# Kernel optimization log

Hardware: AMD Instinct MI355X
Metric: run time of the kernel (lower is better)

## Reference

```python
import jax, jax.numpy as jnp
import numpy as np

H, W = 512, 512          # image_size
N = 10000                # num gaussians (point cloud size)
NUM_VIEWS = 4
PATCH = 40               # original uses arange(v-20, v+20) -> 40px window


def setup_inputs() -> dict:
    key = jax.random.key(0)
    ks = jax.random.split(key, 6)
    means = jax.random.normal(ks[0], (N, 3), dtype=jnp.float32) * 0.5
    log_scales = jnp.log(0.1) + 0.1 * jax.random.normal(ks[1], (N, 3), dtype=jnp.float32)
    q = jax.random.normal(ks[2], (N, 4), dtype=jnp.float32)
    quats = q / jnp.linalg.norm(q, axis=1, keepdims=True)
    shs = jax.random.normal(ks[3], (N, 3, 16), dtype=jnp.float32) * 0.1  # (sh_degree+1)^2 = 16
    opacities = jnp.full((N, 1), 0.5, dtype=jnp.float32)
    # Camera poses: small yaw sweep looking at the origin from z=+5 so points project in-frame.
    poses = []
    for a in np.linspace(-0.1, 0.1, NUM_VIEWS):
        Rm = np.array([[np.cos(a), 0.0, np.sin(a)],
                       [0.0, 1.0, 0.0],
                       [-np.sin(a), 0.0, np.cos(a)]], dtype=np.float32)
        P = np.eye(4, dtype=np.float32)
        P[:3, :3] = Rm
        P[:3, 3] = np.array([0.0, 0.0, 5.0], dtype=np.float32)
        poses.append(P)
    poses = jnp.asarray(np.stack(poses))
    intrinsics = jnp.asarray(np.array([[500.0, 0.0, 256.0],
                                       [0.0, 500.0, 256.0],
                                       [0.0, 0.0, 1.0]], dtype=np.float32))
    return {"poses": poses, "intrinsics": intrinsics, "means": means,
            "log_scales": log_scales, "quats": quats, "shs": shs, "opacities": opacities}


def _quat_to_mat(q):
    # q: (N,4) wxyz -> (N,3,3), same formula as the torch module
    w, x, y, z = q[:, 0], q[:, 1], q[:, 2], q[:, 3]
    r0 = jnp.stack([1 - 2 * (y * y + z * z), 2 * (x * y - w * z), 2 * (x * z + w * y)], -1)
    r1 = jnp.stack([2 * (x * y + w * z), 1 - 2 * (x * x + z * z), 2 * (y * z - w * x)], -1)
    r2 = jnp.stack([2 * (x * z - w * y), 2 * (y * z + w * x), 1 - 2 * (x * x + y * y)], -1)
    return jnp.stack([r0, r1, r2], -2)


def _render_view(pose, K, means, log_scales, quats, shs, opacities):
    Rm = pose[:3, :3]
    t = pose[:3, 3]
    p_cam = means @ Rm.T + t                      # (N,3)
    p_proj = p_cam @ K.T                          # (N,3)
    uv = p_proj[:, :2] / (p_proj[:, 2:3] + 1e-8)  # (N,2)
    u = jnp.trunc(uv[:, 0]).astype(jnp.int32)     # int(uv) truncation as in python int()
    v = jnp.trunc(uv[:, 1]).astype(jnp.int32)
    valid = (p_cam[:, 2] >= 0.1) & (u >= 0) & (u < W) & (v >= 0) & (v < H)

    scales = jnp.exp(log_scales)                  # (N,3); module uses scale (not scale^2)
    Rg = _quat_to_mat(quats)                      # (N,3,3)
    cov = jnp.einsum('nij,nj,nkj->nik', Rg, scales, Rg)  # R diag(s) R^T
    a, b = cov[:, 0, 0], cov[:, 0, 1]
    c, d = cov[:, 1, 0], cov[:, 1, 1]
    det = a * d - b * c
    inv = jnp.stack([jnp.stack([d, -b], -1), jnp.stack([-c, a], -1)], -2) / det[:, None, None]  # inverse of cov[:2,:2]

    off = jnp.arange(PATCH, dtype=jnp.int32) - PATCH // 2  # -20..19, matches arange(v-20, v+20)
    yy = jnp.broadcast_to(v[:, None, None] + off[None, :, None], (N, PATCH, PATCH))
    xx = jnp.broadcast_to(u[:, None, None] + off[None, None, :], (N, PATCH, PATCH))
    pos = jnp.stack([xx, yy], -1).astype(jnp.float32) - uv[:, None, None, :]  # (N,40,40,2)
    expo = -0.5 * jnp.einsum('nyxi,nij,nyxj->nyx', pos, inv, pos)
    g = jnp.exp(jnp.clip(expo, -10.0, 0.0))

    inb = (yy >= 0) & (yy < H) & (xx >= 0) & (xx < W)
    mask = valid[:, None, None] & inb & (g > 0.001)

    color = jax.nn.sigmoid(shs[:, :, 0])          # (N,3)
    op = jax.nn.sigmoid(opacities)                # (N,1)
    contrib = jnp.where(mask, g, 0.0)[..., None] * (op * color)[:, None, None, :]  # (N,40,40,3)

    image = jnp.zeros((H, W, 3), jnp.float32)
    image = image.at[jnp.clip(yy, 0, H - 1), jnp.clip(xx, 0, W - 1)].add(contrib)
    return image


def reference(poses, intrinsics, means, log_scales, quats, shs, opacities):
    # loop over a small fixed number of views (matches forward's per-view loop)
    imgs = [_render_view(poses[i], intrinsics, means, log_scales, quats, shs, opacities)
            for i in range(NUM_VIEWS)]
    return jnp.stack(imgs)  # (num_views, H, W, 3)
```

## Files before the change

kernel.cpp:

```cpp
#include <hip/hip_runtime.h>

#define IMG_H 512
#define IMG_W 512
#define NGAUSS 10000
#define N_VIEWS 4
#define PATCH 40
#define TOTAL_G (N_VIEWS * NGAUSS)

#define QMAX 13.815511f

struct __align__(16) Desc {
    float uvx, uvy, i00, i01;
    float i11, w0, w1, w2;
    int xlo, ylo, wx, area;
};

__global__ __launch_bounds__(256) void gs_prep_kernel(
    const float* __restrict__ poses,
    const float* __restrict__ Km,
    const float* __restrict__ means,
    const float* __restrict__ log_scales,
    const float* __restrict__ quats,
    const float* __restrict__ shs,
    const float* __restrict__ opac,
    Desc* __restrict__ descs,
    float4* __restrict__ out4, int n4)
{
    const int tid = blockIdx.x * 256 + threadIdx.x;

    for (int i = tid; i < n4; i += gridDim.x * 256)
        out4[i] = make_float4(0.f, 0.f, 0.f, 0.f);

    if (tid >= TOTAL_G) return;
    const int view = tid / NGAUSS;
    const int n    = tid - view * NGAUSS;

    const float* P = poses + view * 16;
    const float m0 = means[n * 3 + 0];
    const float m1 = means[n * 3 + 1];
    const float m2 = means[n * 3 + 2];

    const float Xc = P[0] * m0 + P[1] * m1 + P[2]  * m2 + P[3];
    const float Yc = P[4] * m0 + P[5] * m1 + P[6]  * m2 + P[7];
    const float Zc = P[8] * m0 + P[9] * m1 + P[10] * m2 + P[11];

    const float ppx = Km[0] * Xc + Km[1] * Yc + Km[2] * Zc;
    const float ppy = Km[3] * Xc + Km[4] * Yc + Km[5] * Zc;
    const float ppz = Km[6] * Xc + Km[7] * Yc + Km[8] * Zc;

    const float denom = ppz + 1e-8f;
    const float uvx = ppx / denom;
    const float uvy = ppy / denom;

    const int u = (int)uvx;
    const int v = (int)uvy;

    Desc d;
    d.area = 0;

    if ((Zc >= 0.1f) && (u >= 0) && (u < IMG_W) && (v >= 0) && (v < IMG_H)) {
        const float qw = quats[n * 4 + 0];
        const float qx = quats[n * 4 + 1];
        const float qy = quats[n * 4 + 2];
        const float qz = quats[n * 4 + 3];
        const float R00 = 1.0f - 2.0f * (qy * qy + qz * qz);
        const float R01 = 2.0f * (qx * qy - qw * qz);
        const float R02 = 2.0f * (qx * qz + qw * qy);
        const float R10 = 2.0f * (qx * qy + qw * qz);
        const float R11 = 1.0f - 2.0f * (qx * qx + qz * qz);
        const float R12 = 2.0f * (qy * qz - qw * qx);

        const float s0 = expf(log_scales[n * 3 + 0]);
        const float s1 = expf(log_scales[n * 3 + 1]);
        const float s2 = expf(log_scales[n * 3 + 2]);

        const float a = R00 * R00 * s0 + R01 * R01 * s1 + R02 * R02 * s2;
        const float b = R00 * R10 * s0 + R01 * R11 * s1 + R02 * R12 * s2;
        const float dd = R10 * R10 * s0 + R11 * R11 * s1 + R12 * R12 * s2;

        const float det = a * dd - b * b;
        d.i00 =  dd / det;
        d.i01 = -b  / det;
        d.i11 =  a  / det;

        const float rx = sqrtf(QMAX * a)  + 0.5f;
        const float ry = sqrtf(QMAX * dd) + 0.5f;

        int xlo = (int)ceilf (uvx - rx);
        int xhi = (int)floorf(uvx + rx);
        int ylo = (int)ceilf (uvy - ry);
        int yhi = (int)floorf(uvy + ry);
        xlo = max(xlo, max(u - PATCH / 2, 0));
        xhi = min(xhi, min(u + PATCH / 2 - 1, IMG_W - 1));
        ylo = max(ylo, max(v - PATCH / 2, 0));
        yhi = min(yhi, min(v + PATCH / 2 - 1, IMG_H - 1));

        const int wx = xhi - xlo + 1;
        const int wy = yhi - ylo + 1;
        if (wx > 0 && wy > 0) {
            const float op = 1.0f / (1.0f + expf(-opac[n]));
            d.w0 = op / (1.0f + expf(-shs[n * 48 +  0]));
            d.w1 = op / (1.0f + expf(-shs[n * 48 + 16]));
            d.w2 = op / (1.0f + expf(-shs[n * 48 + 32]));
            d.uvx = uvx; d.uvy = uvy;
            d.xlo = xlo; d.ylo = ylo; d.wx = wx;
            d.area = wx * wy;
        }
    }

    if (d.area == 0) {
        d.uvx = d.uvy = d.i00 = d.i01 = d.i11 = d.w0 = d.w1 = d.w2 = 0.f;
        d.xlo = d.ylo = d.wx = 0;
    }
    descs[tid] = d;
}

__global__ __launch_bounds__(256) void gs_splat_kernel(
    const Desc* __restrict__ descs,
    float* __restrict__ out)
{
    const int gtid = blockIdx.x * 256 + threadIdx.x;
    const int sid  = gtid >> 5;
    if (sid >= TOTAL_G) return;
    const int sub  = threadIdx.x & 31;

    const Desc d = descs[sid];
    if (d.area == 0) return;

    const int view = sid / NGAUSS;
    float* img = out + (size_t)view * IMG_H * IMG_W * 3;

    for (int p = sub; p < d.area; p += 32) {
        const int iy = p / d.wx;
        const int ix = p - iy * d.wx;
        const int yy = d.ylo + iy;
        const int xx = d.xlo + ix;

        const float dx = (float)xx - d.uvx;
        const float dy = (float)yy - d.uvy;
        const float q  = dx * (d.i00 * dx + d.i01 * dy) + dy * (d.i01 * dx + d.i11 * dy);
        float expo = -0.5f * q;
        expo = fminf(fmaxf(expo, -10.0f), 0.0f);
        const float g = expf(expo);

        if (g > 0.001f) {
            float* pp = img + ((size_t)yy * IMG_W + xx) * 3;
            atomicAdd(pp + 0, g * d.w0);
            atomicAdd(pp + 1, g * d.w1);
            atomicAdd(pp + 2, g * d.w2);
        }
    }
}

extern "C" void kernel_launch(void* const* d_in, const int* in_sizes, int n_in,
                              void* d_out, int out_size, void* d_ws, size_t ws_size,
                              hipStream_t stream) {
    const float* poses      = (const float*)d_in[0];
    const float* intrinsics = (const float*)d_in[1];
    const float* means      = (const float*)d_in[2];
    const float* log_scales = (const float*)d_in[3];
    const float* quats      = (const float*)d_in[4];
    const float* shs        = (const float*)d_in[5];
    const float* opac       = (const float*)d_in[6];
    float* out  = (float*)d_out;
    Desc* descs = (Desc*)d_ws;

    const int n4 = out_size / 4;
    const int prep_blocks = (n4 + 255) / 256;
    gs_prep_kernel<<<prep_blocks, 256, 0, stream>>>(
        poses, intrinsics, means, log_scales, quats, shs, opac,
        descs, (float4*)out, n4);

    const int splat_blocks = (TOTAL_G * 32 + 255) / 256;
    gs_splat_kernel<<<splat_blocks, 256, 0, stream>>>(descs, out);
}
```

Before: 93.76 us.

## Replace atomic scatter splatting with tile-binned per-pixel gather

Bins each Gaussian into the 16x16 screen tiles its footprint overlaps, building per-tile index lists with atomic counters in the prep kernel. A gather kernel then runs one block per tile, stages descriptors in shared memory, accumulates colour in registers, and writes each pixel once. This removes the output zero-fill and the per-pixel float atomics to global memory. In exchange, lists are capped at a fixed 2048 entries per tile, which can silently drop contributions in dense tiles, and work per tile may be heavily imbalanced.

After: 127.0 us. +35.5%, slower.

```diff
diff --git a/kernel.cpp b/kernel.cpp
--- a/kernel.cpp
+++ b/kernel.cpp
@@ -7,12 +7,19 @@
 #define PATCH 40
 #define TOTAL_G (N_VIEWS * NGAUSS)
 
+#define TILE 16
+#define TILES_X (IMG_W / TILE)
+#define TILES_Y (IMG_H / TILE)
+#define TILES_PER_VIEW (TILES_X * TILES_Y)
+#define NTILES (N_VIEWS * TILES_PER_VIEW)
+#define CAP 2048
+
 #define QMAX 13.815511f
 
 struct __align__(16) Desc {
     float uvx, uvy, i00, i01;
     float i11, w0, w1, w2;
-    int xlo, ylo, wx, area;
+    int   xlo, ylo, xhi, yhi;
 };
 
 __global__ __launch_bounds__(256) void gs_prep_kernel(
@@ -24,13 +31,10 @@
     const float* __restrict__ shs,
     const float* __restrict__ opac,
     Desc* __restrict__ descs,
-    float4* __restrict__ out4, int n4)
+    int* __restrict__ counts,
+    int* __restrict__ lists)
 {
     const int tid = blockIdx.x * 256 + threadIdx.x;
-
-    for (int i = tid; i < n4; i += gridDim.x * 256)
-        out4[i] = make_float4(0.f, 0.f, 0.f, 0.f);
-
     if (tid >= TOTAL_G) return;
     const int view = tid / NGAUSS;
     const int n    = tid - view * NGAUSS;
@@ -55,101 +59,125 @@
     const int u = (int)uvx;
     const int v = (int)uvy;
 
+    if (!((Zc >= 0.1f) && (u >= 0) && (u < IMG_W) && (v >= 0) && (v < IMG_H)))
+        return;
+
+    const float qw = quats[n * 4 + 0];
+    const float qx = quats[n * 4 + 1];
+    const float qy = quats[n * 4 + 2];
+    const float qz = quats[n * 4 + 3];
+    const float R00 = 1.0f - 2.0f * (qy * qy + qz * qz);
+    const float R01 = 2.0f * (qx * qy - qw * qz);
+    const float R02 = 2.0f * (qx * qz + qw * qy);
+    const float R10 = 2.0f * (qx * qy + qw * qz);
+    const float R11 = 1.0f - 2.0f * (qx * qx + qz * qz);
+    const float R12 = 2.0f * (qy * qz - qw * qx);
+
+    const float s0 = expf(log_scales[n * 3 + 0]);
+    const float s1 = expf(log_scales[n * 3 + 1]);
+    const float s2 = expf(log_scales[n * 3 + 2]);
+
+    const float a  = R00 * R00 * s0 + R01 * R01 * s1 + R02 * R02 * s2;
+    const float b  = R00 * R10 * s0 + R01 * R11 * s1 + R02 * R12 * s2;
+    const float dd = R10 * R10 * s0 + R11 * R11 * s1 + R12 * R12 * s2;
+
+    const float det = a * dd - b * b;
+
+    const float rx = sqrtf(QMAX * a)  + 0.5f;
+    const float ry = sqrtf(QMAX * dd) + 0.5f;
+
+    int xlo = (int)ceilf (uvx - rx);
+    int xhi = (int)floorf(uvx + rx);
+    int ylo = (int)ceilf (uvy - ry);
+    int yhi = (int)floorf(uvy + ry);
+    xlo = max(xlo, max(u - PATCH / 2, 0));
+    xhi = min(xhi, min(u + PATCH / 2 - 1, IMG_W - 1));
+    ylo = max(ylo, max(v - PATCH / 2, 0));
+    yhi = min(yhi, min(v + PATCH / 2 - 1, IMG_H - 1));
+    if (xhi < xlo || yhi < ylo) return;
+
+    const float op = 1.0f / (1.0f + expf(-opac[n]));
+
     Desc d;
-    d.area = 0;
-
-    if ((Zc >= 0.1f) && (u >= 0) && (u < IMG_W) && (v >= 0) && (v < IMG_H)) {
-        const float qw = quats[n * 4 + 0];
-        const float qx = quats[n * 4 + 1];
-        const float qy = quats[n * 4 + 2];
-        const float qz = quats[n * 4 + 3];
-        const float R00 = 1.0f - 2.0f * (qy * qy + qz * qz);
-        const float R01 = 2.0f * (qx * qy - qw * qz);
-        const float R02 = 2.0f * (qx * qz + qw * qy);
-        const float R10 = 2.0f * (qx * qy + qw * qz);
-        const float R11 = 1.0f - 2.0f * (qx * qx + qz * qz);
-        const float R12 = 2.0f * (qy * qz - qw * qx);
-
-        const float s0 = expf(log_scales[n * 3 + 0]);
-        const float s1 = expf(log_scales[n * 3 + 1]);
-        const float s2 = expf(log_scales[n * 3 + 2]);
-
-        const float a = R00 * R00 * s0 + R01 * R01 * s1 + R02 * R02 * s2;
-        const float b = R00 * R10 * s0 + R01 * R11 * s1 + R02 * R12 * s2;
-        const float dd = R10 * R10 * s0 + R11 * R11 * s1 + R12 * R12 * s2;
-
-        const float det = a * dd - b * b;
-        d.i00 =  dd / det;
-        d.i01 = -b  / det;
-        d.i11 =  a  / det;
-
-        const float rx = sqrtf(QMAX * a)  + 0.5f;
-        const float ry = sqrtf(QMAX * dd) + 0.5f;
-
-        int xlo = (int)ceilf (uvx - rx);
-        int xhi = (int)floorf(uvx + rx);
-        int ylo = (int)ceilf (uvy - ry);
-        int yhi = (int)floorf(uvy + ry);
-        xlo = max(xlo, max(u - PATCH / 2, 0));
-        xhi = min(xhi, min(u + PATCH / 2 - 1, IMG_W - 1));
-        ylo = max(ylo, max(v - PATCH / 2, 0));
-        yhi = min(yhi, min(v + PATCH / 2 - 1, IMG_H - 1));
-
-        const int wx = xhi - xlo + 1;
-        const int wy = yhi - ylo + 1;
-        if (wx > 0 && wy > 0) {
-            const float op = 1.0f / (1.0f + expf(-opac[n]));
-            d.w0 = op / (1.0f + expf(-shs[n * 48 +  0]));
-            d.w1 = op / (1.0f + expf(-shs[n * 48 + 16]));
-            d.w2 = op / (1.0f + expf(-shs[n * 48 + 32]));
-            d.uvx = uvx; d.uvy = uvy;
-            d.xlo = xlo; d.ylo = ylo; d.wx = wx;
-            d.area = wx * wy;
+    d.uvx = uvx; d.uvy = uvy;
+    d.i00 =  dd / det;
+    d.i01 = -b  / det;
+    d.i11 =  a  / det;
+    d.w0  = op / (1.0f + expf(-shs[n * 48 +  0]));
+    d.w1  = op / (1.0f + expf(-shs[n * 48 + 16]));
+    d.w2  = op / (1.0f + expf(-shs[n * 48 + 32]));
+    d.xlo = xlo; d.ylo = ylo; d.xhi = xhi; d.yhi = yhi;
+    descs[tid] = d;
+
+    const int tx0 = xlo >> 4, tx1 = xhi >> 4;
+    const int ty0 = ylo >> 4, ty1 = yhi >> 4;
+    for (int ty = ty0; ty <= ty1; ++ty) {
+        for (int tx = tx0; tx <= tx1; ++tx) {
+            const int t = view * TILES_PER_VIEW + ty * TILES_X + tx;
+            const int idx = atomicAdd(&counts[t], 1);
+            if (idx < CAP) lists[(size_t)t * CAP + idx] = tid;
         }
     }
-
-    if (d.area == 0) {
-        d.uvx = d.uvy = d.i00 = d.i01 = d.i11 = d.w0 = d.w1 = d.w2 = 0.f;
-        d.xlo = d.ylo = d.wx = 0;
-    }
-    descs[tid] = d;
 }
 
-__global__ __launch_bounds__(256) void gs_splat_kernel(
+__global__ __launch_bounds__(256) void gs_gather_kernel(
     const Desc* __restrict__ descs,
+    const int*  __restrict__ counts,
+    const int*  __restrict__ lists,
     float* __restrict__ out)
 {
-    const int gtid = blockIdx.x * 256 + threadIdx.x;
-    const int sid  = gtid >> 5;
-    if (sid >= TOTAL_G) return;
-    const int sub  = threadIdx.x & 31;
-
-    const Desc d = descs[sid];
-    if (d.area == 0) return;
-
-    const int view = sid / NGAUSS;
-    float* img = out + (size_t)view * IMG_H * IMG_W * 3;
-
-    for (int p = sub; p < d.area; p += 32) {
-        const int iy = p / d.wx;
-        const int ix = p - iy * d.wx;
-        const int yy = d.ylo + iy;
-        const int xx = d.xlo + ix;
-
-        const float dx = (float)xx - d.uvx;
-        const float dy = (float)yy - d.uvy;
-        const float q  = dx * (d.i00 * dx + d.i01 * dy) + dy * (d.i01 * dx + d.i11 * dy);
-        float expo = -0.5f * q;
-        expo = fminf(fmaxf(expo, -10.0f), 0.0f);
-        const float g = expf(expo);
-
-        if (g > 0.001f) {
-            float* pp = img + ((size_t)yy * IMG_W + xx) * 3;
-            atomicAdd(pp + 0, g * d.w0);
-            atomicAdd(pp + 1, g * d.w1);
-            atomicAdd(pp + 2, g * d.w2);
+    __shared__ float4 sd[64][3];
+
+    const int b    = blockIdx.x;
+    const int view = b >> 10;
+    const int tile = b & (TILES_PER_VIEW - 1);
+    const int ty   = tile >> 5;
+    const int tx   = tile & (TILES_X - 1);
+    const int px   = (tx << 4) + (threadIdx.x & 15);
+    const int py   = (ty << 4) + (threadIdx.x >> 4);
+
+    int c = counts[b];
+    if (c > CAP) c = CAP;
+    const int* lst = lists + (size_t)b * CAP;
+
+    float r0 = 0.f, r1 = 0.f, r2 = 0.f;
+    const float fx = (float)px, fy = (float)py;
+
+    for (int base = 0; base < c; base += 64) {
+        const int m = min(64, c - base);
+        if ((int)threadIdx.x < m) {
+            const float4* dp = (const float4*)&descs[lst[base + threadIdx.x]];
+            sd[threadIdx.x][0] = dp[0];
+            sd[threadIdx.x][1] = dp[1];
+            sd[threadIdx.x][2] = dp[2];
         }
+        __syncthreads();
+        for (int j = 0; j < m; ++j) {
+            const float4 f2 = sd[j][2];
+            const int xlo = __float_as_int(f2.x);
+            const int ylo = __float_as_int(f2.y);
+            const int xhi = __float_as_int(f2.z);
+            const int yhi = __float_as_int(f2.w);
+            if (px < xlo || px > xhi || py < ylo || py > yhi) continue;
+
+            const float4 f0 = sd[j][0];
+            const float dx = fx - f0.x;
+            const float dy = fy - f0.y;
+            const float4 f1 = sd[j][1];
+            const float q  = dx * (f0.z * dx + f0.w * dy) + dy * (f0.w * dx + f1.x * dy);
+            float expo = fminf(fmaxf(-0.5f * q, -10.0f), 0.0f);
+            const float g = expf(expo);
+            if (g > 0.001f) {
+                r0 += g * f1.y;
+                r1 += g * f1.z;
+                r2 += g * f1.w;
+            }
+        }
+        __syncthreads();
     }
+
+    float* pp = out + (((size_t)view * IMG_H + py) * IMG_W + px) * 3;
+    pp[0] = r0; pp[1] = r1; pp[2] = r2;
 }
 
 extern "C" void kernel_launch(void* const* d_in, const int* in_sizes, int n_in,
@@ -162,15 +190,17 @@
     const float* quats      = (const float*)d_in[4];
     const float* shs        = (const float*)d_in[5];
     const float* opac       = (const float*)d_in[6];
-    float* out  = (float*)d_out;
-    Desc* descs = (Desc*)d_ws;
-
-    const int n4 = out_size / 4;
-    const int prep_blocks = (n4 + 255) / 256;
-    gs_prep_kernel<<<prep_blocks, 256, 0, stream>>>(
-        poses, intrinsics, means, log_scales, quats, shs, opac,
-        descs, (float4*)out, n4);
-
-    const int splat_blocks = (TOTAL_G * 32 + 255) / 256;
-    gs_splat_kernel<<<splat_blocks, 256, 0, stream>>>(descs, out);
+    float* out = (float*)d_out;
+
+    char* ws = (char*)d_ws;
+    Desc* descs  = (Desc*)ws;
+    int*  counts = (int*)(ws + (size_t)TOTAL_G * sizeof(Desc));
+    int*  lists  = (int*)(ws + (size_t)TOTAL_G * sizeof(Desc) + (size_t)NTILES * sizeof(int));
+
+    hipMemsetAsync(counts, 0, (size_t)NTILES * sizeof(int), stream);
+
+    gs_prep_kernel<<<(TOTAL_G + 255) / 256, 256, 0, stream>>>(
+        poses, intrinsics, means, log_scales, quats, shs, opac, descs, counts, lists);
+
+    gs_gather_kernel<<<NTILES, 256, 0, stream>>>(descs, counts, lists, out);
 }
```
